# Kernel tuning notes

Hardware: AMD Instinct MI355X
Metric: run time of the kernel (lower is better)

Reference implementation:

```python
import jax, jax.numpy as jnp
import numpy as np

B, Q, D = 4, 1024, 1024
N, DH = 16, 64  # n_head, d_head
SCALE = 1.0 / DH ** 0.5
LN_EPS = 1e-5


def setup_inputs() -> dict:
    key = jax.random.key(0)
    ks = jax.random.split(key, 10)
    return {
        "w": jax.random.normal(ks[0], (B, Q, D), jnp.float32),
        "r_emb": jax.random.normal(ks[1], (Q, N, DH), jnp.float32),
        "r_w_bias": jax.random.normal(ks[2], (N, DH), jnp.float32),
        "r_bias": jax.random.normal(ks[3], (Q, N), jnp.float32),
        # projection weights stored [in, out]; torch Linear init std = 1/sqrt(d_head)
        "Wq": jax.random.normal(ks[4], (D, N * DH), jnp.float32) * SCALE,
        "Wk": jax.random.normal(ks[5], (D, N * DH), jnp.float32) * SCALE,
        "Wv": jax.random.normal(ks[6], (D, N * DH), jnp.float32) * SCALE,
        "Wo": jax.random.normal(ks[7], (N * DH, D), jnp.float32) * SCALE,
        "ln_gamma": jnp.ones((D,), jnp.float32),
        "ln_beta": jnp.zeros((D,), jnp.float32),
    }


def _rel_shift(x):
    # x: [b, i, j, n]; pad a zero column at the end of j then drop j=0
    # equivalent to shifting left by one along j with a trailing zero.
    return jnp.concatenate([x[:, :, 1:, :], jnp.zeros_like(x[:, :, :1, :])], axis=2)


def reference(w, r_emb, r_w_bias, r_bias, Wq, Wk, Wv, Wo, ln_gamma, ln_beta):
    b, qlen, d = w.shape
    klen = qlen  # mems=None
    n, dh = r_w_bias.shape

    q_h = (w @ Wq).reshape(b, qlen, n, dh)
    k_h = (w @ Wk).reshape(b, klen, n, dh)
    v_h = (w @ Wv).reshape(b, klen, n, dh)

    rw_q = q_h + r_w_bias[None, None]                      # [b,q,n,dh]
    AC = jnp.einsum('bind,bjnd->bijn', rw_q, k_h)          # [b,q,k,n]
    B_ = jnp.einsum('bind,jnd->bijn', q_h, r_emb)          # [b,q,k,n]
    BD = _rel_shift(B_ + r_bias[None, None])               # [b,q,k,n]

    attn_score = (AC + BD) * SCALE
    attn_prob = jax.nn.softmax(attn_score, axis=2)
    attn_vec = jnp.einsum('bijn,bjnd->bind', attn_prob, v_h)
    attn_out = attn_vec.reshape(b, qlen, n * dh) @ Wo

    out = w + attn_out  # residual (post-lnorm path)
    mu = jnp.mean(out, axis=-1, keepdims=True)
    var = jnp.var(out, axis=-1, keepdims=True)
    return (out - mu) / jnp.sqrt(var + LN_EPS) * ln_gamma + ln_beta
```

## Files before the change

kernel.cpp:

```cpp
#include <hip/hip_runtime.h>
#include <hip/hip_bf16.h>

using f16 = _Float16;
typedef _Float16 f16x8 __attribute__((ext_vector_type(8)));
typedef _Float16 f16x4 __attribute__((ext_vector_type(4)));
typedef float f32x4 __attribute__((ext_vector_type(4)));

#define AS1 __attribute__((address_space(1)))
#define AS3 __attribute__((address_space(3)))

constexpr int Bc = 4, Qc = 1024, Dc = 1024, Nh = 16, DHc = 64;
constexpr int BQ = Bc * Qc;
constexpr int NHEAD = Bc * Nh;
constexpr float ATT_SCALE = 0.125f;
constexpr float LOG2E = 1.44269504088896f;

struct Ptr4 { const float* p[4]; };
__global__ __launch_bounds__(256) void k_prep(
    const float* __restrict__ w_in, f16* __restrict__ wh,
    Ptr4 srcs, f16* __restrict__ WT,
    const float* __restrict__ remb, f16* __restrict__ Ke)
{
    const int bid = blockIdx.x, tid = threadIdx.x;
    if (bid < 2048) {
        long i8 = ((long)bid * 256 + tid) * 8;
        float4 a = *(const float4*)&w_in[i8];
        float4 b = *(const float4*)&w_in[i8 + 4];
        f16x8 o = { (f16)a.x, (f16)a.y, (f16)a.z, (f16)a.w,
                    (f16)b.x, (f16)b.y, (f16)b.z, (f16)b.w };
        *(f16x8*)&wh[i8] = o;
    } else if (bid < 6144) {
        __shared__ f16 tile[32][33];
        int idx = bid - 2048;
        int z = idx >> 10, rem = idx & 1023;
        int r0 = (rem >> 5) * 32, c0 = (rem & 31) * 32;
        const float* src = srcs.p[z];
        f16* d = WT + (long)z * Dc * Dc;
        int tx = tid & 31, ty = tid >> 5;
#pragma unroll
        for (int dy = 0; dy < 32; dy += 8) {
            int r = r0 + ty + dy, c = c0 + tx;
            tile[ty + dy][tx] = (f16)src[(long)r * Dc + c];
        }
        __syncthreads();
#pragma unroll
        for (int dy = 0; dy < 32; dy += 8) {
            int c = c0 + ty + dy, r = r0 + tx;
            d[(long)c * Dc + r] = tile[tx][ty + dy];
        }
    } else {
        long gid = (long)(bid - 6144) * 256 + tid;
        int d8 = (int)(gid & 7) * 8;
        int j = (int)((gid >> 3) & 1023);
        int h = (int)(gid >> 13);
        int n = h & 15;
        f16x8 kv;
        if (j < 1023) {
            const float* rp = &remb[((long)(j + 1) * 16 + n) * 64 + d8];
            float4 r0 = *(const float4*)rp, r1 = *(const float4*)(rp + 4);
            kv[0] = (f16)r0.x; kv[1] = (f16)r0.y; kv[2] = (f16)r0.z; kv[3] = (f16)r0.w;
            kv[4] = (f16)r1.x; kv[5] = (f16)r1.y; kv[6] = (f16)r1.z; kv[7] = (f16)r1.w;
        } else {
            kv = f16x8{};
        }
        *(f16x8*)&Ke[(((long)h << 10) + j) * 64 + d8] = kv;
    }
}

template <int BM, int BN, int BK, int WROWS, int WCOLS, int EPI>
__global__ __launch_bounds__(256) void k_gemm_nt(
    const f16* __restrict__ A, const f16* __restrict__ Bt, void* __restrict__ Cv,
    f16* __restrict__ qtp, f16* __restrict__ ktp, f16* __restrict__ vtp,
    int lda, int ldb, int ldc, int K)
{
    static_assert(BK == 64, "geometry below assumes BK=64");
    constexpr int TM = BM / (WROWS * 16);
    constexpr int TN = BN / (WCOLS * 16);
    __shared__ __align__(16) f16 sA[BM * 64];
    __shared__ __align__(16) f16 sB[BN * 64];

    const int tid = threadIdx.x;
    const int lane = tid & 63, wave = tid >> 6;
    const int wm = wave / WCOLS, wn = wave % WCOLS;

    const int nwg = gridDim.x * gridDim.y;
    const int flat = blockIdx.y * gridDim.x + blockIdx.x;
    const int cpx = nwg >> 3;
    const int swz = (flat & 7) * cpx + (flat >> 3);
    const int bx = swz % gridDim.x, by = swz / gridDim.x;
    const int m0 = by * BM, n0 = bx * BN;

    f32x4 acc[TM][TN] = {};

    const int lrow = lane & 15;
    const int quad = lane >> 4;
    const int srow = lane >> 3;
    const int scol = ((lane & 7) ^ (srow & 7)) * 8;

    for (int k0 = 0; k0 < K; k0 += 64) {
        __syncthreads();
        constexpr int CHA = BM / 8;
#pragma unroll
        for (int ch = 0; ch < CHA / 4; ++ch) {
            int cc = ch * 4 + wave;
            __builtin_amdgcn_global_load_lds(
                (const AS1 void*)(const void*)&A[(long)(m0 + cc * 8 + srow) * lda + k0 + scol],
                (AS3 void*)(void*)&sA[cc * 512], 16, 0, 0);
        }
        constexpr int CHB = BN / 8;
#pragma unroll
        for (int ch = 0; ch < CHB / 4; ++ch) {
            int cc = ch * 4 + wave;
            __builtin_amdgcn_global_load_lds(
                (const AS1 void*)(const void*)&Bt[(long)(n0 + cc * 8 + srow) * ldb + k0 + scol],
                (AS3 void*)(void*)&sB[cc * 512], 16, 0, 0);
        }
        __syncthreads();

#pragma unroll
        for (int kk = 0; kk < 2; ++kk) {
            const int kcb = kk * 4 + quad;
            f16x8 af[TM], bfr[TN];
#pragma unroll
            for (int mi = 0; mi < TM; ++mi) {
                int R = wm * TM * 16 + mi * 16 + lrow;
                af[mi] = *(const f16x8*)&sA[R * 64 + ((kcb ^ (lrow & 7)) * 8)];
            }
#pragma unroll
            for (int ni = 0; ni < TN; ++ni) {
                int R = wn * TN * 16 + ni * 16 + lrow;
                bfr[ni] = *(const f16x8*)&sB[R * 64 + ((kcb ^ (lrow & 7)) * 8)];
            }
#pragma unroll
            for (int mi = 0; mi < TM; ++mi)
#pragma unroll
                for (int ni = 0; ni < TN; ++ni)
                    acc[mi][ni] = __builtin_amdgcn_mfma_f32_16x16x32_f16(af[mi], bfr[ni], acc[mi][ni], 0, 0, 0);
        }
    }

    const int crow = (lane >> 4) * 4;
    const int ccol = lane & 15;
#pragma unroll
    for (int mi = 0; mi < TM; ++mi)
#pragma unroll
        for (int ni = 0; ni < TN; ++ni)
#pragma unroll
            for (int r = 0; r < 4; ++r) {
                int gm = m0 + wm * TM * 16 + mi * 16 + crow + r;
                int gn = n0 + wn * TN * 16 + ni * 16 + ccol;
                float val = acc[mi][ni][r];
                if constexpr (EPI == 0) {
                    ((f16*)Cv)[(long)gm * ldc + gn] = (f16)val;
                } else {
                    int seg = n0 >> 10;
                    int col = gn & 1023;
                    if (seg == 0) {
                        qtp[(long)gm * 1024 + col] = (f16)val;
                    } else if (seg == 1) {
                        ktp[(long)gm * 1024 + col] = (f16)val;
                    } else {
                        int b = gm >> 10, i = gm & 1023;
                        vtp[(((long)(b << 10) + col) << 10) + i] = (f16)val;
                    }
                }
            }
}

__global__ __launch_bounds__(512, 4) void k_flash(
    const f16* __restrict__ qh, const f16* __restrict__ kh,
    const f16* __restrict__ Ke, const f16* __restrict__ vT,
    const float* __restrict__ rwb, const float* __restrict__ r_bias,
    f16* __restrict__ avp)
{
    __shared__ __align__(16) f16 sKa[2][64 * 64];
    __shared__ __align__(16) f16 sKe[2][64 * 64];
    __shared__ __align__(16) f16 sVa[2][64 * 64];
    __shared__ float sRB[2][64];

    const int tid = threadIdx.x, lane = tid & 63, wave = tid >> 6;
    const int bid = blockIdx.x;
    const int h = (((bid >> 3) & 7) << 3) | (bid & 7);
    const int i0 = (bid >> 6) * 128;
    const int b = h >> 4, n = h & 15;

    const int lrow = lane & 15;
    const int quad = lane >> 4;
    const int lr3 = lane >> 3;
    const int swc = (lane & 7) ^ (lr3 & 7);

    const f16* srcK = kh + ((long)(b * Qc) + 8 * wave + lr3) * 1024 + n * 64 + swc * 8;
    const f16* srcE = Ke + ((long)h * Qc + 8 * wave + lr3) * 64 + swc * 8;
    const f16* srcV = vT + (long)h * DHc * Qc + (long)(8 * wave + lr3) * Qc + swc * 8;

    f16x8 rw0, rw1;
#pragma unroll
    for (int e = 0; e < 8; ++e) {
        rw0[e] = (f16)(rwb[n * 64 + quad * 8 + e] * ATT_SCALE);
        rw1[e] = (f16)(rwb[n * 64 + 32 + quad * 8 + e] * ATT_SCALE);
    }

    const f16 qsc = (f16)0.125f;
    f16x8 aq[4];
    {
        long rix = (long)(b * Qc + i0 + wave * 16 + lrow) * 1024 + n * 64;
        f16x8 q0 = *(const f16x8*)&qh[rix + quad * 8] * qsc;
        f16x8 q1 = *(const f16x8*)&qh[rix + 32 + quad * 8] * qsc;
        aq[0] = q0 + rw0;
        aq[1] = q1 + rw1;
        aq[2] = q0;
        aq[3] = q1;
    }

    float m_i = -1e30f, l_i = 0.0f;
    f32x4 o_acc[4] = {};

    {
        float rbv = 0.0f;
        if (tid < 64) rbv = r_bias[(tid + 1) * Nh + n] * (ATT_SCALE * LOG2E);
        __builtin_amdgcn_global_load_lds((const AS1 void*)srcK, (AS3 void*)&sKa[0][wave * 512], 16, 0, 0);
        __builtin_amdgcn_global_load_lds((const AS1 void*)srcE, (AS3 void*)&sKe[0][wave * 512], 16, 0, 0);
        __builtin_amdgcn_global_load_lds((const AS1 void*)srcV, (AS3 void*)&sVa[0][wave * 512], 16, 0, 0);
        if (tid < 64) sRB[0][tid] = rbv;
    }
    __syncthreads();

    for (int jt = 0; jt < 16; ++jt) {
        const int cur = jt & 1;

        float rbn = 0.0f;
        if (jt < 15) {
            const int j0n = (jt + 1) * 64;
            __builtin_amdgcn_global_load_lds((const AS1 void*)(srcK + (long)j0n * 1024),
                                             (AS3 void*)&sKa[cur ^ 1][wave * 512], 16, 0, 0);
            __builtin_amdgcn_global_load_lds((const AS1 void*)(srcE + (long)j0n * 64),
                                             (AS3 void*)&sKe[cur ^ 1][wave * 512], 16, 0, 0);
            __builtin_amdgcn_global_load_lds((const AS1 void*)(srcV + j0n),
                                             (AS3 void*)&sVa[cur ^ 1][wave * 512], 16, 0, 0);
            if (tid < 64) {
                int j = j0n + tid;
                rbn = (j < Qc - 1) ? r_bias[(j + 1) * Nh + n] * (ATT_SCALE * LOG2E) : 0.0f;
            }
        }

        const f16* Ka = &sKa[cur][0];
        const f16* Kb = &sKe[cur][0];
        const f16* Va = &sVa[cur][0];
        const int rsw = lrow & 7;

        f32x4 s_acc[4] = {};
#pragma unroll
        for (int ni = 0; ni < 4; ++ni) {
            int rb_ = (ni * 16 + lrow) * 64;
            f16x8 a0 = *(const f16x8*)&Ka[rb_ + ((0 + quad) ^ rsw) * 8];
            f16x8 a1 = *(const f16x8*)&Ka[rb_ + ((4 + quad) ^ rsw) * 8];
            f16x8 e0 = *(const f16x8*)&Kb[rb_ + ((0 + quad) ^ rsw) * 8];
            f16x8 e1 = *(const f16x8*)&Kb[rb_ + ((4 + quad) ^ rsw) * 8];
            s_acc[ni] = __builtin_amdgcn_mfma_f32_16x16x32_f16(a0, aq[0], s_acc[ni], 0, 0, 0);
            s_acc[ni] = __builtin_amdgcn_mfma_f32_16x16x32_f16(a1, aq[1], s_acc[ni], 0, 0, 0);
            s_acc[ni] = __builtin_amdgcn_mfma_f32_16x16x32_f16(e0, aq[2], s_acc[ni], 0, 0, 0);
            s_acc[ni] = __builtin_amdgcn_mfma_f32_16x16x32_f16(e1, aq[3], s_acc[ni], 0, 0, 0);
        }

        f16x4 pf[4];
        float mx = -1e30f, sm = 0.0f;
#pragma unroll
        for (int ni = 0; ni < 4; ++ni) {
            f32x4 rb4 = *(const f32x4*)&sRB[cur][ni * 16 + quad * 4];
            f16x4 pvv;
#pragma unroll
            for (int r = 0; r < 4; ++r) {
                float v = fmaf(s_acc[ni][r], LOG2E, rb4[r]);
                s_acc[ni][r] = v;
                mx = fmaxf(mx, v);
                float e = __builtin_amdgcn_exp2f(v - m_i);
                sm += e;
                pvv[r] = (f16)e;
            }
            pf[ni] = pvv;
        }
        if (!__all(mx - m_i <= 8.0f)) {
            float wmx = fmaxf(mx, __shfl_xor(mx, 16));
            wmx = fmaxf(wmx, __shfl_xor(wmx, 32));
            float mn = fmaxf(m_i, wmx);
            float alpha = __builtin_amdgcn_exp2f(m_i - mn);
            sm = 0.0f;
#pragma unroll
            for (int ni = 0; ni < 4; ++ni) {
                f16x4 pvv;
#pragma unroll
                for (int r = 0; r < 4; ++r) {
                    float e = __builtin_amdgcn_exp2f(s_acc[ni][r] - mn);
                    sm += e;
                    pvv[r] = (f16)e;
                }
                pf[ni] = pvv;
            }
            l_i *= alpha;
#pragma unroll
            for (int r = 0; r < 4; ++r) {
                float al = __shfl(alpha, quad * 4 + r);
#pragma unroll
                for (int dt = 0; dt < 4; ++dt) o_acc[dt][r] *= al;
            }
            m_i = mn;
        }
        l_i += sm;

#pragma unroll
        for (int nj = 0; nj < 4; ++nj) {
            int coff = ((2 * nj + (quad >> 1)) ^ rsw) * 8 + (quad & 1) * 4;
#pragma unroll
            for (int dt = 0; dt < 4; ++dt) {
                f16x4 bv = *(const f16x4*)&Va[(dt * 16 + lrow) * 64 + coff];
                o_acc[dt] = __builtin_amdgcn_mfma_f32_16x16x16f16(pf[nj], bv, o_acc[dt], 0, 0, 0);
            }
        }

        if (jt < 15) {
            if (tid < 64) sRB[cur ^ 1][tid] = rbn;
            __syncthreads();
        }
    }

    l_i += __shfl_xor(l_i, 16);
    l_i += __shfl_xor(l_i, 32);
    {
        float linv = 1.0f / l_i;
#pragma unroll
        for (int r = 0; r < 4; ++r) {
            float li = __shfl(linv, quad * 4 + r);
            int i = i0 + wave * 16 + quad * 4 + r;
#pragma unroll
            for (int dt = 0; dt < 4; ++dt) {
                int d = dt * 16 + lrow;
                avp[((long)(b * Qc + i) << 10) + n * 64 + d] = (f16)(o_acc[dt][r] * li);
            }
        }
    }
}

__global__ __launch_bounds__(256) void k_res_ln(const float* __restrict__ w, const f16* __restrict__ ao,
                                                const float* __restrict__ gamma, const float* __restrict__ beta,
                                                float* __restrict__ out) {
    const long base = (long)blockIdx.x * 1024;
    const int tid = threadIdx.x;
    float4 wv = *(const float4*)&w[base + tid * 4];
    f16x4 av = *(const f16x4*)&ao[base + tid * 4];
    float x[4] = { wv.x + (float)av[0], wv.y + (float)av[1],
                   wv.z + (float)av[2], wv.w + (float)av[3] };
    float s = x[0] + x[1] + x[2] + x[3];
    float s2 = x[0] * x[0] + x[1] * x[1] + x[2] * x[2] + x[3] * x[3];
#pragma unroll
    for (int off = 32; off; off >>= 1) { s += __shfl_down(s, off); s2 += __shfl_down(s2, off); }
    __shared__ float rs[4], rs2[4];
    if ((tid & 63) == 0) { rs[tid >> 6] = s; rs2[tid >> 6] = s2; }
    __syncthreads();
    s = rs[0] + rs[1] + rs[2] + rs[3];
    s2 = rs2[0] + rs2[1] + rs2[2] + rs2[3];
    float mu = s * (1.0f / 1024.0f);
    float var = s2 * (1.0f / 1024.0f) - mu * mu;
    float inv = rsqrtf(var + 1e-5f);
    float4 gv = *(const float4*)&gamma[tid * 4];
    float4 bv = *(const float4*)&beta[tid * 4];
    float4 o;
    o.x = (x[0] - mu) * inv * gv.x + bv.x;
    o.y = (x[1] - mu) * inv * gv.y + bv.y;
    o.z = (x[2] - mu) * inv * gv.z + bv.z;
    o.w = (x[3] - mu) * inv * gv.w + bv.w;
    *(float4*)&out[base + tid * 4] = o;
}

extern "C" void kernel_launch(void* const* d_in, const int* in_sizes, int n_in,
                              void* d_out, int out_size, void* d_ws, size_t ws_size,
                              hipStream_t stream) {
    const float* w_in   = (const float*)d_in[0];
    const float* r_emb  = (const float*)d_in[1];
    const float* r_wb   = (const float*)d_in[2];
    const float* r_bias = (const float*)d_in[3];
    const float* Wq     = (const float*)d_in[4];
    const float* Wk     = (const float*)d_in[5];
    const float* Wv     = (const float*)d_in[6];
    const float* Wo     = (const float*)d_in[7];
    const float* ln_g   = (const float*)d_in[8];
    const float* ln_b   = (const float*)d_in[9];
    float* out = (float*)d_out;

    char* p = (char*)d_ws;
    auto alloc = [&](size_t bytes) { char* r = p; p += (bytes + 255) & ~(size_t)255; return r; };
    f16* wh = (f16*)alloc((size_t)BQ * Dc * 2);
    f16* WT = (f16*)alloc((size_t)4 * Dc * Dc * 2);
    f16* qh = (f16*)alloc((size_t)BQ * Dc * 2);
    f16* kh = (f16*)alloc((size_t)BQ * Dc * 2);
    f16* Ke = (f16*)alloc((size_t)NHEAD * Qc * DHc * 2);
    f16* vT = (f16*)alloc((size_t)BQ * Dc * 2);
    f16* WoT = WT + (size_t)3 * Dc * Dc;
    f16* avp = wh;
    f16* ao  = Ke;

    Ptr4 srcs{{Wq, Wk, Wv, Wo}};
    k_prep<<<8192, 256, 0, stream>>>(w_in, wh, srcs, WT, r_emb, Ke);

    k_gemm_nt<128, 128, 64, 2, 2, 5><<<dim3(3 * Dc / 128, BQ / 128), 256, 0, stream>>>(
        wh, WT, nullptr, qh, kh, vT, Dc, Dc, 0, Dc);

    k_flash<<<512, 512, 0, stream>>>(qh, kh, Ke, vT, r_wb, r_bias, avp);

    k_gemm_nt<64, 128, 64, 2, 2, 0><<<dim3(Dc / 128, BQ / 64), 256, 0, stream>>>(
        avp, WoT, ao, nullptr, nullptr, nullptr, Dc, Dc, Dc, Dc);

    k_res_ln<<<BQ, 256, 0, stream>>>(w_in, ao, ln_g, ln_b, out);
}
```

Baseline: 199.7 us.

## Process two query tiles per wave in flash attention to reuse K/V tiles

Each wave now handles 32 query rows (two 16-row tiles) instead of 16, so every K, Ke and V fragment read from LDS feeds twice as many MFMAs. The block covers 256 query rows, the grid is halved to 256 blocks, and the block-to-(head, query chunk) mapping is reordered. The intent is to cut per-query global and LDS traffic for K/V. In exchange it doubles accumulator registers, lowers the occupancy target to 2 blocks per CU, and leaves fewer blocks than the GPU has CUs, so some CUs may sit idle.

```diff
diff --git a/kernel.cpp b/kernel.cpp
--- a/kernel.cpp
+++ b/kernel.cpp
@@ -167,7 +167,7 @@
             }
 }
 
-__global__ __launch_bounds__(512, 4) void k_flash(
+__global__ __launch_bounds__(512, 2) void k_flash(
     const f16* __restrict__ qh, const f16* __restrict__ kh,
     const f16* __restrict__ Ke, const f16* __restrict__ vT,
     const float* __restrict__ rwb, const float* __restrict__ r_bias,
@@ -180,8 +180,8 @@
 
     const int tid = threadIdx.x, lane = tid & 63, wave = tid >> 6;
     const int bid = blockIdx.x;
-    const int h = (((bid >> 3) & 7) << 3) | (bid & 7);
-    const int i0 = (bid >> 6) * 128;
+    const int h = (bid & 7) * 8 + ((bid >> 3) >> 2);
+    const int i0 = ((bid >> 3) & 3) * 256;
     const int b = h >> 4, n = h & 15;
 
     const int lrow = lane & 15;
@@ -201,19 +201,21 @@
     }
 
     const f16 qsc = (f16)0.125f;
-    f16x8 aq[4];
-    {
-        long rix = (long)(b * Qc + i0 + wave * 16 + lrow) * 1024 + n * 64;
+    f16x8 aq[2][4];
+#pragma unroll
+    for (int t = 0; t < 2; ++t) {
+        long rix = (long)(b * Qc + i0 + wave * 32 + t * 16 + lrow) * 1024 + n * 64;
         f16x8 q0 = *(const f16x8*)&qh[rix + quad * 8] * qsc;
         f16x8 q1 = *(const f16x8*)&qh[rix + 32 + quad * 8] * qsc;
-        aq[0] = q0 + rw0;
-        aq[1] = q1 + rw1;
-        aq[2] = q0;
-        aq[3] = q1;
-    }
-
-    float m_i = -1e30f, l_i = 0.0f;
-    f32x4 o_acc[4] = {};
+        aq[t][0] = q0 + rw0;
+        aq[t][1] = q1 + rw1;
+        aq[t][2] = q0;
+        aq[t][3] = q1;
+    }
+
+    float m_i[2] = {-1e30f, -1e30f};
+    float l_i[2] = {0.0f, 0.0f};
+    f32x4 o_acc[2][4] = {};
 
     {
         float rbv = 0.0f;
@@ -248,7 +250,7 @@
         const f16* Va = &sVa[cur][0];
         const int rsw = lrow & 7;
 
-        f32x4 s_acc[4] = {};
+        f32x4 s_acc[2][4] = {};
 #pragma unroll
         for (int ni = 0; ni < 4; ++ni) {
             int rb_ = (ni * 16 + lrow) * 64;
@@ -256,56 +258,66 @@
             f16x8 a1 = *(const f16x8*)&Ka[rb_ + ((4 + quad) ^ rsw) * 8];
             f16x8 e0 = *(const f16x8*)&Kb[rb_ + ((0 + quad) ^ rsw) * 8];
             f16x8 e1 = *(const f16x8*)&Kb[rb_ + ((4 + quad) ^ rsw) * 8];
-            s_acc[ni] = __builtin_amdgcn_mfma_f32_16x16x32_f16(a0, aq[0], s_acc[ni], 0, 0, 0);
-            s_acc[ni] = __builtin_amdgcn_mfma_f32_16x16x32_f16(a1, aq[1], s_acc[ni], 0, 0, 0);
-            s_acc[ni] = __builtin_amdgcn_mfma_f32_16x16x32_f16(e0, aq[2], s_acc[ni], 0, 0, 0);
-            s_acc[ni] = __builtin_amdgcn_mfma_f32_16x16x32_f16(e1, aq[3], s_acc[ni], 0, 0, 0);
-        }
-
-        f16x4 pf[4];
-        float mx = -1e30f, sm = 0.0f;
-#pragma unroll
-        for (int ni = 0; ni < 4; ++ni) {
-            f32x4 rb4 = *(const f32x4*)&sRB[cur][ni * 16 + quad * 4];
-            f16x4 pvv;
-#pragma unroll
-            for (int r = 0; r < 4; ++r) {
-                float v = fmaf(s_acc[ni][r], LOG2E, rb4[r]);
-                s_acc[ni][r] = v;
-                mx = fmaxf(mx, v);
-                float e = __builtin_amdgcn_exp2f(v - m_i);
-                sm += e;
-                pvv[r] = (f16)e;
-            }
-            pf[ni] = pvv;
-        }
-        if (!__all(mx - m_i <= 8.0f)) {
-            float wmx = fmaxf(mx, __shfl_xor(mx, 16));
-            wmx = fmaxf(wmx, __shfl_xor(wmx, 32));
-            float mn = fmaxf(m_i, wmx);
-            float alpha = __builtin_amdgcn_exp2f(m_i - mn);
-            sm = 0.0f;
+#pragma unroll
+            for (int t = 0; t < 2; ++t) {
+                s_acc[t][ni] = __builtin_amdgcn_mfma_f32_16x16x32_f16(a0, aq[t][0], s_acc[t][ni], 0, 0, 0);
+                s_acc[t][ni] = __builtin_amdgcn_mfma_f32_16x16x32_f16(a1, aq[t][1], s_acc[t][ni], 0, 0, 0);
+                s_acc[t][ni] = __builtin_amdgcn_mfma_f32_16x16x32_f16(e0, aq[t][2], s_acc[t][ni], 0, 0, 0);
+                s_acc[t][ni] = __builtin_amdgcn_mfma_f32_16x16x32_f16(e1, aq[t][3], s_acc[t][ni], 0, 0, 0);
+            }
+        }
+
+        f16x4 pf[2][4];
+        float mx[2] = {-1e30f, -1e30f}, sm[2] = {0.0f, 0.0f};
+#pragma unroll
+        for (int t = 0; t < 2; ++t)
 #pragma unroll
             for (int ni = 0; ni < 4; ++ni) {
+                f32x4 rb4 = *(const f32x4*)&sRB[cur][ni * 16 + quad * 4];
                 f16x4 pvv;
 #pragma unroll
                 for (int r = 0; r < 4; ++r) {
-                    float e = __builtin_amdgcn_exp2f(s_acc[ni][r] - mn);
-                    sm += e;
+                    float v = fmaf(s_acc[t][ni][r], LOG2E, rb4[r]);
+                    s_acc[t][ni][r] = v;
+                    mx[t] = fmaxf(mx[t], v);
+                    float e = __builtin_amdgcn_exp2f(v - m_i[t]);
+                    sm[t] += e;
                     pvv[r] = (f16)e;
                 }
-                pf[ni] = pvv;
-            }
-            l_i *= alpha;
-#pragma unroll
-            for (int r = 0; r < 4; ++r) {
-                float al = __shfl(alpha, quad * 4 + r);
-#pragma unroll
-                for (int dt = 0; dt < 4; ++dt) o_acc[dt][r] *= al;
-            }
-            m_i = mn;
-        }
-        l_i += sm;
+                pf[t][ni] = pvv;
+            }
+        bool ok = (mx[0] - m_i[0] <= 8.0f) && (mx[1] - m_i[1] <= 8.0f);
+        if (!__all(ok)) {
+#pragma unroll
+            for (int t = 0; t < 2; ++t) {
+                float wmx = fmaxf(mx[t], __shfl_xor(mx[t], 16));
+                wmx = fmaxf(wmx, __shfl_xor(wmx, 32));
+                float mn = fmaxf(m_i[t], wmx);
+                float alpha = __builtin_amdgcn_exp2f(m_i[t] - mn);
+                sm[t] = 0.0f;
+#pragma unroll
+                for (int ni = 0; ni < 4; ++ni) {
+                    f16x4 pvv;
+#pragma unroll
+                    for (int r = 0; r < 4; ++r) {
+                        float e = __builtin_amdgcn_exp2f(s_acc[t][ni][r] - mn);
+                        sm[t] += e;
+                        pvv[r] = (f16)e;
+                    }
+                    pf[t][ni] = pvv;
+                }
+                l_i[t] *= alpha;
+#pragma unroll
+                for (int r = 0; r < 4; ++r) {
+                    float al = __shfl(alpha, quad * 4 + r);
+#pragma unroll
+                    for (int dt = 0; dt < 4; ++dt) o_acc[t][dt][r] *= al;
+                }
+                m_i[t] = mn;
+            }
+        }
+        l_i[0] += sm[0];
+        l_i[1] += sm[1];
 
 #pragma unroll
         for (int nj = 0; nj < 4; ++nj) {
@@ -313,7 +325,8 @@
 #pragma unroll
             for (int dt = 0; dt < 4; ++dt) {
                 f16x4 bv = *(const f16x4*)&Va[(dt * 16 + lrow) * 64 + coff];
-                o_acc[dt] = __builtin_amdgcn_mfma_f32_16x16x16f16(pf[nj], bv, o_acc[dt], 0, 0, 0);
+                o_acc[0][dt] = __builtin_amdgcn_mfma_f32_16x16x16f16(pf[0][nj], bv, o_acc[0][dt], 0, 0, 0);
+                o_acc[1][dt] = __builtin_amdgcn_mfma_f32_16x16x16f16(pf[1][nj], bv, o_acc[1][dt], 0, 0, 0);
             }
         }
 
@@ -323,18 +336,20 @@
         }
     }
 
-    l_i += __shfl_xor(l_i, 16);
-    l_i += __shfl_xor(l_i, 32);
-    {
-        float linv = 1.0f / l_i;
+#pragma unroll
+    for (int t = 0; t < 2; ++t) {
+        float lt = l_i[t];
+        lt += __shfl_xor(lt, 16);
+        lt += __shfl_xor(lt, 32);
+        float linv = 1.0f / lt;
 #pragma unroll
         for (int r = 0; r < 4; ++r) {
             float li = __shfl(linv, quad * 4 + r);
-            int i = i0 + wave * 16 + quad * 4 + r;
+            int i = i0 + wave * 32 + t * 16 + quad * 4 + r;
 #pragma unroll
             for (int dt = 0; dt < 4; ++dt) {
                 int d = dt * 16 + lrow;
-                avp[((long)(b * Qc + i) << 10) + n * 64 + d] = (f16)(o_acc[dt][r] * li);
+                avp[((long)(b * Qc + i) << 10) + n * 64 + d] = (f16)(o_acc[t][dt][r] * li);
             }
         }
     }
@@ -404,7 +419,7 @@
     k_gemm_nt<128, 128, 64, 2, 2, 5><<<dim3(3 * Dc / 128, BQ / 128), 256, 0, stream>>>(
         wh, WT, nullptr, qh, kh, vT, Dc, Dc, 0, Dc);
 
-    k_flash<<<512, 512, 0, stream>>>(qh, kh, Ke, vT, r_wb, r_bias, avp);
+    k_flash<<<256, 512, 0, stream>>>(qh, kh, Ke, vT, r_wb, r_bias, avp);
 
     k_gemm_nt<64, 128, 64, 2, 2, 0><<<dim3(Dc / 128, BQ / 64), 256, 0, stream>>>(
         avp, WoT, ao, nullptr, nullptr, nullptr, Dc, Dc, Dc, Dc);
```

Result: slower. 209.4 us (+4.9%).

## Fold positional keys and r_w_bias into K and per-key bias in GEMM epilogue

Applied to the files above, without the earlier changes.

Rewrites the score as q·(k+e_shifted) + r_w_bias·k + r_bias. The QKV GEMM epilogue now stores k+Ke as the key tensor and writes a per-head, per-key scalar bias. The attention kernel then needs only two MFMAs per key tile instead of four, and no longer streams the separate positional-key tile through LDS. In exchange the projection epilogue does extra reads, a shuffle reduction and an extra bias buffer write, and k+e is rounded to f16 once.

```diff
diff --git a/kernel.cpp b/kernel.cpp
--- a/kernel.cpp
+++ b/kernel.cpp
@@ -71,6 +71,8 @@
 __global__ __launch_bounds__(256) void k_gemm_nt(
     const f16* __restrict__ A, const f16* __restrict__ Bt, void* __restrict__ Cv,
     f16* __restrict__ qtp, f16* __restrict__ ktp, f16* __restrict__ vtp,
+    const float* __restrict__ rwb, const float* __restrict__ rbias,
+    const f16* __restrict__ KeAdd, float* __restrict__ ckrb,
     int lda, int ldb, int ldc, int K)
 {
     static_assert(BK == 64, "geometry below assumes BK=64");
@@ -141,6 +143,45 @@
 
     const int crow = (lane >> 4) * 4;
     const int ccol = lane & 15;
+
+    if constexpr (EPI == 5) {
+        int seg = n0 >> 10;
+        if (seg == 1) {
+            const int hn = ((n0 & 1023) + wn * TN * 16) >> 6;
+            float rwbl[TN];
+#pragma unroll
+            for (int ni = 0; ni < TN; ++ni)
+                rwbl[ni] = rwb[hn * 64 + ni * 16 + ccol];
+#pragma unroll
+            for (int mi = 0; mi < TM; ++mi)
+#pragma unroll
+                for (int r = 0; r < 4; ++r) {
+                    int gm = m0 + wm * TM * 16 + mi * 16 + crow + r;
+                    int bb = gm >> 10, j = gm & 1023;
+                    long kebase = (((long)(bb * 16 + hn) << 10) + j) * 64;
+                    float dot = 0.0f;
+#pragma unroll
+                    for (int ni = 0; ni < TN; ++ni) {
+                        float val = acc[mi][ni][r];
+                        dot += val * rwbl[ni];
+                        int d = ni * 16 + ccol;
+                        ktp[(long)gm * 1024 + hn * 64 + d] =
+                            (f16)(val + (float)KeAdd[kebase + d]);
+                    }
+                    dot += __shfl_xor(dot, 1);
+                    dot += __shfl_xor(dot, 2);
+                    dot += __shfl_xor(dot, 4);
+                    dot += __shfl_xor(dot, 8);
+                    if (ccol == 0) {
+                        float rbv = (j < 1023) ? rbias[(j + 1) * 16 + hn] : 0.0f;
+                        ckrb[(((long)(bb * 16 + hn)) << 10) + j] =
+                            (dot + rbv) * (ATT_SCALE * LOG2E);
+                    }
+                }
+            return;
+        }
+    }
+
 #pragma unroll
     for (int mi = 0; mi < TM; ++mi)
 #pragma unroll
@@ -157,8 +198,6 @@
                     int col = gn & 1023;
                     if (seg == 0) {
                         qtp[(long)gm * 1024 + col] = (f16)val;
-                    } else if (seg == 1) {
-                        ktp[(long)gm * 1024 + col] = (f16)val;
                     } else {
                         int b = gm >> 10, i = gm & 1023;
                         vtp[(((long)(b << 10) + col) << 10) + i] = (f16)val;
@@ -169,12 +208,10 @@
 
 __global__ __launch_bounds__(512, 4) void k_flash(
     const f16* __restrict__ qh, const f16* __restrict__ kh,
-    const f16* __restrict__ Ke, const f16* __restrict__ vT,
-    const float* __restrict__ rwb, const float* __restrict__ r_bias,
+    const f16* __restrict__ vT, const float* __restrict__ ckrb,
     f16* __restrict__ avp)
 {
     __shared__ __align__(16) f16 sKa[2][64 * 64];
-    __shared__ __align__(16) f16 sKe[2][64 * 64];
     __shared__ __align__(16) f16 sVa[2][64 * 64];
     __shared__ float sRB[2][64];
 
@@ -190,26 +227,14 @@
     const int swc = (lane & 7) ^ (lr3 & 7);
 
     const f16* srcK = kh + ((long)(b * Qc) + 8 * wave + lr3) * 1024 + n * 64 + swc * 8;
-    const f16* srcE = Ke + ((long)h * Qc + 8 * wave + lr3) * 64 + swc * 8;
     const f16* srcV = vT + (long)h * DHc * Qc + (long)(8 * wave + lr3) * Qc + swc * 8;
 
-    f16x8 rw0, rw1;
-#pragma unroll
-    for (int e = 0; e < 8; ++e) {
-        rw0[e] = (f16)(rwb[n * 64 + quad * 8 + e] * ATT_SCALE);
-        rw1[e] = (f16)(rwb[n * 64 + 32 + quad * 8 + e] * ATT_SCALE);
-    }
-
     const f16 qsc = (f16)0.125f;
-    f16x8 aq[4];
+    f16x8 aq[2];
     {
         long rix = (long)(b * Qc + i0 + wave * 16 + lrow) * 1024 + n * 64;
-        f16x8 q0 = *(const f16x8*)&qh[rix + quad * 8] * qsc;
-        f16x8 q1 = *(const f16x8*)&qh[rix + 32 + quad * 8] * qsc;
-        aq[0] = q0 + rw0;
-        aq[1] = q1 + rw1;
-        aq[2] = q0;
-        aq[3] = q1;
+        aq[0] = *(const f16x8*)&qh[rix + quad * 8] * qsc;
+        aq[1] = *(const f16x8*)&qh[rix + 32 + quad * 8] * qsc;
     }
 
     float m_i = -1e30f, l_i = 0.0f;
@@ -217,9 +242,8 @@
 
     {
         float rbv = 0.0f;
-        if (tid < 64) rbv = r_bias[(tid + 1) * Nh + n] * (ATT_SCALE * LOG2E);
+        if (tid < 64) rbv = ckrb[((long)h << 10) + tid];
         __builtin_amdgcn_global_load_lds((const AS1 void*)srcK, (AS3 void*)&sKa[0][wave * 512], 16, 0, 0);
-        __builtin_amdgcn_global_load_lds((const AS1 void*)srcE, (AS3 void*)&sKe[0][wave * 512], 16, 0, 0);
         __builtin_amdgcn_global_load_lds((const AS1 void*)srcV, (AS3 void*)&sVa[0][wave * 512], 16, 0, 0);
         if (tid < 64) sRB[0][tid] = rbv;
     }
@@ -233,18 +257,12 @@
             const int j0n = (jt + 1) * 64;
             __builtin_amdgcn_global_load_lds((const AS1 void*)(srcK + (long)j0n * 1024),
                                              (AS3 void*)&sKa[cur ^ 1][wave * 512], 16, 0, 0);
-            __builtin_amdgcn_global_load_lds((const AS1 void*)(srcE + (long)j0n * 64),
-                                             (AS3 void*)&sKe[cur ^ 1][wave * 512], 16, 0, 0);
             __builtin_amdgcn_global_load_lds((const AS1 void*)(srcV + j0n),
                                              (AS3 void*)&sVa[cur ^ 1][wave * 512], 16, 0, 0);
-            if (tid < 64) {
-                int j = j0n + tid;
-                rbn = (j < Qc - 1) ? r_bias[(j + 1) * Nh + n] * (ATT_SCALE * LOG2E) : 0.0f;
-            }
+            if (tid < 64) rbn = ckrb[((long)h << 10) + j0n + tid];
         }
 
         const f16* Ka = &sKa[cur][0];
-        const f16* Kb = &sKe[cur][0];
         const f16* Va = &sVa[cur][0];
         const int rsw = lrow & 7;
 
@@ -254,12 +272,8 @@
             int rb_ = (ni * 16 + lrow) * 64;
             f16x8 a0 = *(const f16x8*)&Ka[rb_ + ((0 + quad) ^ rsw) * 8];
             f16x8 a1 = *(const f16x8*)&Ka[rb_ + ((4 + quad) ^ rsw) * 8];
-            f16x8 e0 = *(const f16x8*)&Kb[rb_ + ((0 + quad) ^ rsw) * 8];
-            f16x8 e1 = *(const f16x8*)&Kb[rb_ + ((4 + quad) ^ rsw) * 8];
             s_acc[ni] = __builtin_amdgcn_mfma_f32_16x16x32_f16(a0, aq[0], s_acc[ni], 0, 0, 0);
             s_acc[ni] = __builtin_amdgcn_mfma_f32_16x16x32_f16(a1, aq[1], s_acc[ni], 0, 0, 0);
-            s_acc[ni] = __builtin_amdgcn_mfma_f32_16x16x32_f16(e0, aq[2], s_acc[ni], 0, 0, 0);
-            s_acc[ni] = __builtin_amdgcn_mfma_f32_16x16x32_f16(e1, aq[3], s_acc[ni], 0, 0, 0);
         }
 
         f16x4 pf[4];
@@ -394,6 +408,7 @@
     f16* kh = (f16*)alloc((size_t)BQ * Dc * 2);
     f16* Ke = (f16*)alloc((size_t)NHEAD * Qc * DHc * 2);
     f16* vT = (f16*)alloc((size_t)BQ * Dc * 2);
+    float* ckrb = (float*)alloc((size_t)NHEAD * Qc * 4);
     f16* WoT = WT + (size_t)3 * Dc * Dc;
     f16* avp = wh;
     f16* ao  = Ke;
@@ -402,12 +417,13 @@
     k_prep<<<8192, 256, 0, stream>>>(w_in, wh, srcs, WT, r_emb, Ke);
 
     k_gemm_nt<128, 128, 64, 2, 2, 5><<<dim3(3 * Dc / 128, BQ / 128), 256, 0, stream>>>(
-        wh, WT, nullptr, qh, kh, vT, Dc, Dc, 0, Dc);
-
-    k_flash<<<512, 512, 0, stream>>>(qh, kh, Ke, vT, r_wb, r_bias, avp);
+        wh, WT, nullptr, qh, kh, vT, r_wb, r_bias, Ke, ckrb, Dc, Dc, 0, Dc);
+
+    k_flash<<<512, 512, 0, stream>>>(qh, kh, vT, ckrb, avp);
 
     k_gemm_nt<64, 128, 64, 2, 2, 0><<<dim3(Dc / 128, BQ / 64), 256, 0, stream>>>(
-        avp, WoT, ao, nullptr, nullptr, nullptr, Dc, Dc, Dc, Dc);
+        avp, WoT, ao, nullptr, nullptr, nullptr, nullptr, nullptr, nullptr, nullptr,
+        Dc, Dc, Dc, Dc);
 
     k_res_ln<<<BQ, 256, 0, stream>>>(w_in, ao, ln_g, ln_b, out);
 }
```

After: 211.5 us. +5.9%, slower.
